# Optimization experiments

Hardware: AMD Instinct MI355X
Metric: run time of the kernel (lower is better)

Reference implementation:

```python
import jax, jax.numpy as jnp
import numpy as np

SIGMA_RGB = 15.0   # sigma_rgb init kwarg
WEIGHT = 1.0       # lambda_ init kwarg
# scale_factor = 0.5 is hard-coded via stride-2 nearest / 2x2-mean bilinear downsampling


def setup_inputs() -> dict:
    key = jax.random.key(0)
    k1, k2 = jax.random.split(key)
    B, H, W = 2, 224, 224
    fcams = jax.random.normal(k1, (B, 2, H, W), dtype=jnp.float32)          # seg logits, C=2
    raw_img = jax.random.uniform(k2, (B, 3, H, W), dtype=jnp.float32) * 255.0  # RGB image
    return {"fcams": fcams, "raw_img": raw_img}


def _down_nearest(x):
    # F.interpolate(scale_factor=0.5, mode='nearest') == stride-2 sampling at even indices
    return x[..., ::2, ::2]


def _down_bilinear(x):
    # F.interpolate(scale_factor=0.5, mode='bilinear', align_corners=False):
    # output center maps to input coord 2i+0.5 -> mean of each 2x2 block
    B, C, H, W = x.shape
    return x.reshape(B, C, H // 2, 2, W // 2, 2).mean(axis=(3, 5))


def _crf_energy_single(img, seg):
    # img: [3, h, w], seg: [C, h, w]
    # Dense color-Gaussian pairwise term: sum_{i,j,c} exp(-||f_i-f_j||^2/2) s_ic s_jc
    C = seg.shape[0]
    f = img.reshape(3, -1).T / SIGMA_RGB            # [P, 3] color features
    s = seg.reshape(C, -1).T                        # [P, C]
    sq = jnp.sum(f * f, axis=1)                     # [P]
    D = sq[:, None] + sq[None, :] - 2.0 * (f @ f.T) # [P, P] squared color distances
    K = jnp.exp(-0.5 * D)                           # [P, P] Gaussian affinity
    AS = K @ s                                      # [P, C] filtered segmentations
    return jnp.sum(s * AS)


def reference(fcams, raw_img):
    # fcams.shape[1] > 1 -> softmax over channels
    fcams_n = jax.nn.softmax(fcams, axis=1)
    img_s = _down_nearest(raw_img)     # [B, 3, h, w]
    seg_s = _down_bilinear(fcams_n)    # [B, C, h, w]
    B = raw_img.shape[0]
    # sequential over batch to keep only one [P,P] kernel live at a time
    per = jax.lax.map(lambda t: _crf_energy_single(t[0], t[1]), (img_s, seg_s))
    loss = -jnp.sum(per) / B
    return WEIGHT * loss
```

## Files before the change

### kernel.cpp

```cpp
#include <hip/hip_runtime.h>

#define H 224
#define W 224
#define HOUT 112
#define P 12544
#define PPAD 13312
#define NTILES 13
#define ITILE 1024
#define JCHUNK 64
#define NCHUNKS 196
#define JOBS_PER_BATCH 1300

__device__ __forceinline__ float fast_exp2(float x) {
    return __builtin_amdgcn_exp2f(x);
}

__global__ __launch_bounds__(256) void crf_prep(const float* __restrict__ fcams,
                                                const float* __restrict__ img,
                                                float4* __restrict__ recA,
                                                float* __restrict__ recU) {
    int idx = blockIdx.x * 256 + threadIdx.x;
    int b = idx / PPAD;
    int p = idx - b * PPAD;
    float fx = 0.f, fy = 0.f, fz = 0.f, A = -1e30f, u = 0.f;
    if (p < P) {
        int y = p / HOUT, x = p - y * HOUT;
        const float* ib = img + (size_t)b * 3 * H * W;
        int off = (2 * y) * W + 2 * x;
        const float inv_sigma = 1.0f / 15.0f;
        fx = ib[off] * inv_sigma;
        fy = ib[H * W + off] * inv_sigma;
        fz = ib[2 * H * W + off] * inv_sigma;
        const float c0 = -0.72134752044448170f;
        A = c0 * (fx * fx + fy * fy + fz * fz);
        const float* cb = fcams + (size_t)b * 2 * H * W;
        const float l2e = 1.44269504088896340f;
        float s = 0.f;
        #pragma unroll
        for (int dy = 0; dy < 2; ++dy) {
            #pragma unroll
            for (int dx = 0; dx < 2; ++dx) {
                int o = (2 * y + dy) * W + (2 * x + dx);
                float d = cb[o] - cb[H * W + o];
                s += 1.0f / (1.0f + fast_exp2(-d * l2e));
            }
        }
        u = 0.25f * s;
    }
    recA[idx] = make_float4(fx, fy, fz, A);
    recU[idx] = u;
}

__global__ __launch_bounds__(256) void crf_energy(const float4* __restrict__ recA,
                                                  const float* __restrict__ recU,
                                                  float* __restrict__ out) {
    __shared__ float4 jsA[JCHUNK];
    __shared__ float  jsU[JCHUNK];

    int bid = blockIdx.x;
    int b = bid / JOBS_PER_BATCH;
    int r = bid - b * JOBS_PER_BATCH;
    int it = 0;
    #pragma unroll 1
    for (; it < NTILES; ++it) {
        int cnt = (it < 12) ? (NCHUNKS - 16 * it) : 4;
        if (r < cnt) break;
        r -= cnt;
    }
    int jc = 16 * it + r;
    float scale = (r >= 16) ? 2.0f : 1.0f;

    const float4* baseA = recA + (size_t)b * PPAD;
    const float*  baseU = recU + (size_t)b * PPAD;

    if (threadIdx.x < JCHUNK) {
        jsA[threadIdx.x] = baseA[jc * JCHUNK + threadIdx.x];
        jsU[threadIdx.x] = baseU[jc * JCHUNK + threadIdx.x];
    }

    const float l2e = 1.44269504088896340f;
    float fx2[4], fy2[4], fz2[4], Ai[4], pi[4], qi[4];
    int i0 = it * ITILE + threadIdx.x * 4;
    #pragma unroll
    for (int k = 0; k < 4; ++k) {
        float4 a = baseA[i0 + k];
        float  u = baseU[i0 + k];
        fx2[k] = a.x * l2e; fy2[k] = a.y * l2e; fz2[k] = a.z * l2e;
        Ai[k] = a.w;
        pi[k] = 2.f * u - 1.f;
        qi[k] = 1.f - u;
    }
    __syncthreads();

    float Su[4] = {0.f, 0.f, 0.f, 0.f};
    float S1[4] = {0.f, 0.f, 0.f, 0.f};
    #pragma unroll 4
    for (int j = 0; j < JCHUNK; ++j) {
        float4 a = jsA[j];
        float uj = jsU[j];
        #pragma unroll
        for (int k = 0; k < 4; ++k) {
            float t = Ai[k] + a.w;
            t = fmaf(fx2[k], a.x, t);
            t = fmaf(fy2[k], a.y, t);
            t = fmaf(fz2[k], a.z, t);
            float kx = fast_exp2(t);
            Su[k] = fmaf(kx, uj, Su[k]);
            S1[k] += kx;
        }
    }
    float tot = 0.f;
    #pragma unroll
    for (int k = 0; k < 4; ++k) tot += pi[k] * Su[k] + qi[k] * S1[k];
    tot *= scale;

    #pragma unroll
    for (int o = 32; o > 0; o >>= 1) tot += __shfl_down(tot, o);

    __shared__ float wsum[4];
    int lane = threadIdx.x & 63, wid = threadIdx.x >> 6;
    if (lane == 0) wsum[wid] = tot;
    __syncthreads();
    if (threadIdx.x == 0) {
        atomicAdd(out, -0.5f * ((wsum[0] + wsum[1]) + (wsum[2] + wsum[3])));
    }
}

extern "C" void kernel_launch(void* const* d_in, const int* in_sizes, int n_in,
                              void* d_out, int out_size, void* d_ws, size_t ws_size,
                              hipStream_t stream) {
    const float* fcams = (const float*)d_in[0];
    const float* img   = (const float*)d_in[1];
    float* out = (float*)d_out;

    float4* recA = (float4*)d_ws;
    float*  recU = (float*)((char*)d_ws + 2 * PPAD * sizeof(float4));

    hipMemsetAsync(d_out, 0, sizeof(float), stream);
    crf_prep<<<(2 * PPAD) / 256, 256, 0, stream>>>(fcams, img, recA, recU);
    crf_energy<<<2 * JOBS_PER_BATCH, 256, 0, stream>>>(recA, recU, out);
}
```

Before: 51.46 us.

## Pair-interleave point records to use packed FMA in the pairwise energy loop

The prep kernel now writes point features as interleaved pairs (x0,x1,y0,y1 / z0,z1,A0,A1 / u0,u1), so the energy kernel can evaluate two j points at once with packed 2-wide float add/FMA ops, which the MI355X supports as v_pk_fma_f32. This targets the VALU cost of the exponent argument computation, while the exp2 calls stay scalar. The hipMemsetAsync of the output is dropped and the output is zeroed by thread 0 of the prep kernel, saving one stream operation. Risks include shuffle and move overhead if the compiler does not emit packed instructions, and higher register pressure from the duplicated i-side values.

```diff
diff --git a/kernel.cpp b/kernel.cpp
--- a/kernel.cpp
+++ b/kernel.cpp
@@ -1,13 +1,18 @@
 #include <hip/hip_runtime.h>
+
+typedef float f32x2 __attribute__((ext_vector_type(2)));
+typedef float f32x4 __attribute__((ext_vector_type(4)));
 
 #define H 224
 #define W 224
 #define HOUT 112
 #define P 12544
 #define PPAD 13312
+#define MPB (PPAD/2)
 #define NTILES 13
 #define ITILE 1024
 #define JCHUNK 64
+#define MCHUNK 32
 #define NCHUNKS 196
 #define JOBS_PER_BATCH 1300
 
@@ -15,47 +20,65 @@
     return __builtin_amdgcn_exp2f(x);
 }
 
+__device__ __forceinline__ f32x2 pk_fma(f32x2 a, f32x2 b, f32x2 c) {
+    return __builtin_elementwise_fma(a, b, c);
+}
+__device__ __forceinline__ f32x2 pk_add(f32x2 a, f32x2 b) {
+    return a + b;
+}
+
 __global__ __launch_bounds__(256) void crf_prep(const float* __restrict__ fcams,
                                                 const float* __restrict__ img,
-                                                float4* __restrict__ recA,
-                                                float* __restrict__ recU) {
+                                                f32x4* __restrict__ gA,
+                                                f32x4* __restrict__ gB,
+                                                f32x2* __restrict__ gU,
+                                                float* __restrict__ out) {
     int idx = blockIdx.x * 256 + threadIdx.x;
-    int b = idx / PPAD;
-    int p = idx - b * PPAD;
-    float fx = 0.f, fy = 0.f, fz = 0.f, A = -1e30f, u = 0.f;
-    if (p < P) {
-        int y = p / HOUT, x = p - y * HOUT;
-        const float* ib = img + (size_t)b * 3 * H * W;
-        int off = (2 * y) * W + 2 * x;
-        const float inv_sigma = 1.0f / 15.0f;
-        fx = ib[off] * inv_sigma;
-        fy = ib[H * W + off] * inv_sigma;
-        fz = ib[2 * H * W + off] * inv_sigma;
-        const float c0 = -0.72134752044448170f;
-        A = c0 * (fx * fx + fy * fy + fz * fz);
-        const float* cb = fcams + (size_t)b * 2 * H * W;
-        const float l2e = 1.44269504088896340f;
-        float s = 0.f;
-        #pragma unroll
-        for (int dy = 0; dy < 2; ++dy) {
+    if (idx == 0) out[0] = 0.f;
+    int b = idx / MPB;
+    int m = idx - b * MPB;
+    const float* ib = img + (size_t)b * 3 * H * W;
+    const float* cb = fcams + (size_t)b * 2 * H * W;
+    float fx[2] = {0.f, 0.f}, fy[2] = {0.f, 0.f}, fz[2] = {0.f, 0.f};
+    float Av[2] = {-1e30f, -1e30f}, uv[2] = {0.f, 0.f};
+    #pragma unroll
+    for (int s = 0; s < 2; ++s) {
+        int p = 2 * m + s;
+        if (p < P) {
+            int y = p / HOUT, x = p - y * HOUT;
+            int off = (2 * y) * W + 2 * x;
+            const float inv_sigma = 1.0f / 15.0f;
+            float a0 = ib[off] * inv_sigma;
+            float a1 = ib[H * W + off] * inv_sigma;
+            float a2 = ib[2 * H * W + off] * inv_sigma;
+            fx[s] = a0; fy[s] = a1; fz[s] = a2;
+            Av[s] = -0.72134752044448170f * (a0 * a0 + a1 * a1 + a2 * a2);
+            const float l2e = 1.44269504088896340f;
+            float ssum = 0.f;
             #pragma unroll
-            for (int dx = 0; dx < 2; ++dx) {
-                int o = (2 * y + dy) * W + (2 * x + dx);
-                float d = cb[o] - cb[H * W + o];
-                s += 1.0f / (1.0f + fast_exp2(-d * l2e));
+            for (int dy = 0; dy < 2; ++dy) {
+                #pragma unroll
+                for (int dx = 0; dx < 2; ++dx) {
+                    int o = (2 * y + dy) * W + (2 * x + dx);
+                    float d = cb[o] - cb[H * W + o];
+                    ssum += 1.0f / (1.0f + fast_exp2(-d * l2e));
+                }
             }
+            uv[s] = 0.25f * ssum;
         }
-        u = 0.25f * s;
     }
-    recA[idx] = make_float4(fx, fy, fz, A);
-    recU[idx] = u;
+    f32x4 ra; ra.x = fx[0]; ra.y = fx[1]; ra.z = fy[0]; ra.w = fy[1];
+    f32x4 rb; rb.x = fz[0]; rb.y = fz[1]; rb.z = Av[0]; rb.w = Av[1];
+    f32x2 ru; ru.x = uv[0]; ru.y = uv[1];
+    gA[idx] = ra; gB[idx] = rb; gU[idx] = ru;
 }
 
-__global__ __launch_bounds__(256) void crf_energy(const float4* __restrict__ recA,
-                                                  const float* __restrict__ recU,
+__global__ __launch_bounds__(256) void crf_energy(const f32x4* __restrict__ gA,
+                                                  const f32x4* __restrict__ gB,
+                                                  const f32x2* __restrict__ gU,
                                                   float* __restrict__ out) {
-    __shared__ float4 jsA[JCHUNK];
-    __shared__ float  jsU[JCHUNK];
+    __shared__ f32x4 sA[MCHUNK], sB[MCHUNK];
+    __shared__ f32x2 sU[MCHUNK];
 
     int bid = blockIdx.x;
     int b = bid / JOBS_PER_BATCH;
@@ -70,58 +93,77 @@
     int jc = 16 * it + r;
     float scale = (r >= 16) ? 2.0f : 1.0f;
 
-    const float4* baseA = recA + (size_t)b * PPAD;
-    const float*  baseU = recU + (size_t)b * PPAD;
+    const f32x4* gAb = gA + (size_t)b * MPB;
+    const f32x4* gBb = gB + (size_t)b * MPB;
+    const f32x2* gUb = gU + (size_t)b * MPB;
 
-    if (threadIdx.x < JCHUNK) {
-        jsA[threadIdx.x] = baseA[jc * JCHUNK + threadIdx.x];
-        jsU[threadIdx.x] = baseU[jc * JCHUNK + threadIdx.x];
-    }
+    int t = threadIdx.x;
+    if (t < MCHUNK)              sA[t] = gAb[jc * MCHUNK + t];
+    else if (t < 2 * MCHUNK)     sB[t - MCHUNK] = gBb[jc * MCHUNK + t - MCHUNK];
+    else if (t < 3 * MCHUNK)     sU[t - 2 * MCHUNK] = gUb[jc * MCHUNK + t - 2 * MCHUNK];
 
+    int m0 = it * (ITILE / 2) + t * 2;
+    f32x4 qa0 = gAb[m0], qa1 = gAb[m0 + 1];
+    f32x4 qb0 = gBb[m0], qb1 = gBb[m0 + 1];
+    f32x2 qu0 = gUb[m0], qu1 = gUb[m0 + 1];
     const float l2e = 1.44269504088896340f;
-    float fx2[4], fy2[4], fz2[4], Ai[4], pi[4], qi[4];
-    int i0 = it * ITILE + threadIdx.x * 4;
+    float axv[4] = {qa0.x, qa0.y, qa1.x, qa1.y};
+    float ayv[4] = {qa0.z, qa0.w, qa1.z, qa1.w};
+    float azv[4] = {qb0.x, qb0.y, qb1.x, qb1.y};
+    float Aiv[4] = {qb0.z, qb0.w, qb1.z, qb1.w};
+    float uiv[4] = {qu0.x, qu0.y, qu1.x, qu1.y};
+    f32x2 fxS[4], fyS[4], fzS[4], AiS[4], Su[4], S1[4];
+    float piv[4], qiv[4];
     #pragma unroll
     for (int k = 0; k < 4; ++k) {
-        float4 a = baseA[i0 + k];
-        float  u = baseU[i0 + k];
-        fx2[k] = a.x * l2e; fy2[k] = a.y * l2e; fz2[k] = a.z * l2e;
-        Ai[k] = a.w;
-        pi[k] = 2.f * u - 1.f;
-        qi[k] = 1.f - u;
+        fxS[k].x = fxS[k].y = axv[k] * l2e;
+        fyS[k].x = fyS[k].y = ayv[k] * l2e;
+        fzS[k].x = fzS[k].y = azv[k] * l2e;
+        AiS[k].x = AiS[k].y = Aiv[k];
+        Su[k].x = Su[k].y = 0.f;
+        S1[k].x = S1[k].y = 0.f;
+        piv[k] = 2.f * uiv[k] - 1.f;
+        qiv[k] = 1.f - uiv[k];
     }
     __syncthreads();
 
-    float Su[4] = {0.f, 0.f, 0.f, 0.f};
-    float S1[4] = {0.f, 0.f, 0.f, 0.f};
     #pragma unroll 4
-    for (int j = 0; j < JCHUNK; ++j) {
-        float4 a = jsA[j];
-        float uj = jsU[j];
+    for (int m = 0; m < MCHUNK; ++m) {
+        f32x4 a  = sA[m];
+        f32x4 b4 = sB[m];
+        f32x2 u2 = sU[m];
+        f32x2 ax2 = __builtin_shufflevector(a, a, 0, 1);
+        f32x2 ay2 = __builtin_shufflevector(a, a, 2, 3);
+        f32x2 az2 = __builtin_shufflevector(b4, b4, 0, 1);
+        f32x2 Aj2 = __builtin_shufflevector(b4, b4, 2, 3);
         #pragma unroll
         for (int k = 0; k < 4; ++k) {
-            float t = Ai[k] + a.w;
-            t = fmaf(fx2[k], a.x, t);
-            t = fmaf(fy2[k], a.y, t);
-            t = fmaf(fz2[k], a.z, t);
-            float kx = fast_exp2(t);
-            Su[k] = fmaf(kx, uj, Su[k]);
-            S1[k] += kx;
+            f32x2 t2 = pk_add(Aj2, AiS[k]);
+            t2 = pk_fma(ax2, fxS[k], t2);
+            t2 = pk_fma(ay2, fyS[k], t2);
+            t2 = pk_fma(az2, fzS[k], t2);
+            f32x2 e;
+            e.x = fast_exp2(t2.x);
+            e.y = fast_exp2(t2.y);
+            Su[k] = pk_fma(e, u2, Su[k]);
+            S1[k] = pk_add(S1[k], e);
         }
     }
+
     float tot = 0.f;
     #pragma unroll
-    for (int k = 0; k < 4; ++k) tot += pi[k] * Su[k] + qi[k] * S1[k];
+    for (int k = 0; k < 4; ++k)
+        tot += piv[k] * (Su[k].x + Su[k].y) + qiv[k] * (S1[k].x + S1[k].y);
     tot *= scale;
 
     #pragma unroll
     for (int o = 32; o > 0; o >>= 1) tot += __shfl_down(tot, o);
 
     __shared__ float wsum[4];
-    int lane = threadIdx.x & 63, wid = threadIdx.x >> 6;
+    int lane = t & 63, wid = t >> 6;
     if (lane == 0) wsum[wid] = tot;
     __syncthreads();
-    if (threadIdx.x == 0) {
+    if (t == 0) {
         atomicAdd(out, -0.5f * ((wsum[0] + wsum[1]) + (wsum[2] + wsum[3])));
     }
 }
@@ -133,10 +175,11 @@
     const float* img   = (const float*)d_in[1];
     float* out = (float*)d_out;
 
-    float4* recA = (float4*)d_ws;
-    float*  recU = (float*)((char*)d_ws + 2 * PPAD * sizeof(float4));
+    char* ws = (char*)d_ws;
+    f32x4* gA = (f32x4*)ws;
+    f32x4* gB = (f32x4*)(ws + (size_t)2 * MPB * 16);
+    f32x2* gU = (f32x2*)(ws + (size_t)4 * MPB * 16);
 
-    hipMemsetAsync(d_out, 0, sizeof(float), stream);
-    crf_prep<<<(2 * PPAD) / 256, 256, 0, stream>>>(fcams, img, recA, recU);
-    crf_energy<<<2 * JOBS_PER_BATCH, 256, 0, stream>>>(recA, recU, out);
+    crf_prep<<<(2 * MPB) / 256, 256, 0, stream>>>(fcams, img, gA, gB, gU, out);
+    crf_energy<<<2 * JOBS_PER_BATCH, 256, 0, stream>>>(gA, gB, gU, out);
 }
```

Result: no change. 52.31 us (+1.6%).
